# Optimization experiments

Hardware: AMD Instinct MI355X
Metric: run time of the kernel (lower is better)

Reference implementation:

```python
import jax, jax.numpy as jnp
import numpy as np

NPG = 39      # nodes per graph, from (1+8+64+9)*(39+1)=3280 = lin1 in_features
NEG_SLOPE = 0.2


def gat_conv(x, src, dst, W, a_src, a_dst, b, n):
    """PyG GATConv, heads=1, self-loops already appended to (src, dst).
    x:[N,Fin] W:[Fin,Fout] a_src/a_dst:[Fout] b:[Fout] -> [N,Fout]"""
    h = x @ W                                        # [N,Fout]
    e = jax.nn.leaky_relu(h[src] @ a_src + h[dst] @ a_dst, NEG_SLOPE)  # [E]
    m = jax.lax.stop_gradient(jax.ops.segment_max(e, dst, num_segments=n))
    w = jnp.exp(e - m[dst])
    denom = jax.ops.segment_sum(w, dst, num_segments=n)
    alpha = w / (denom[dst] + 1e-16)                 # segment softmax per target node
    out = jax.ops.segment_sum(alpha[:, None] * h[src], dst, num_segments=n)
    return out + b


def setup_inputs() -> dict:
    key = jax.random.key(0)
    ks = jax.random.split(key, 20)
    B, DEG = 4096, 8
    N = B * NPG
    E = N * DEG
    x = jax.random.normal(ks[0], (N, 1), dtype=jnp.float32)
    # block-diagonal edges: each node emits DEG edges to random nodes in SAME graph
    src = jnp.repeat(jnp.arange(N, dtype=jnp.int64), DEG)
    offs = (src // NPG) * NPG
    dst = offs + jax.random.randint(ks[1], (E,), 0, NPG, dtype=jnp.int64)
    edge_index = jnp.stack([src, dst])
    batch_vec = jnp.repeat(jnp.arange(B, dtype=jnp.int64), NPG)

    def glorot(k, shape):
        fan = shape[0] + (shape[1] if len(shape) > 1 else 1)
        s = jnp.sqrt(6.0 / fan)
        return jax.random.uniform(k, shape, jnp.float32, -s, s)

    p = {
        'W1': glorot(ks[2], (1, 8)),   'a1s': glorot(ks[3], (8,)),  'a1d': glorot(ks[4], (8,)),  'b1': jnp.zeros((8,), jnp.float32),
        'W2': glorot(ks[5], (8, 64)),  'a2s': glorot(ks[6], (64,)), 'a2d': glorot(ks[7], (64,)), 'b2': jnp.zeros((64,), jnp.float32),
        'W3': glorot(ks[8], (64, 9)),  'a3s': glorot(ks[9], (9,)),  'a3d': glorot(ks[10], (9,)), 'b3': jnp.zeros((9,), jnp.float32),
        'lW1': glorot(ks[11], (3280, 5000)), 'lb1': jnp.zeros((5000,), jnp.float32),
        'lW2': glorot(ks[12], (5000, 1024)), 'lb2': jnp.zeros((1024,), jnp.float32),
        'lW3': glorot(ks[13], (1024, 9)),    'lb3': jnp.zeros((9,), jnp.float32),
    }
    return {'x': x, 'edge_index': edge_index, 'batch_vec': batch_vec, **p}


def reference(x, edge_index, batch_vec,
              W1, a1s, a1d, b1, W2, a2s, a2d, b2, W3, a3s, a3d, b3,
              lW1, lb1, lW2, lb2, lW3, lb3):
    N = x.shape[0]
    B = N // NPG
    loops = jnp.arange(N, dtype=edge_index.dtype)
    src = jnp.concatenate([edge_index[0], loops])   # GATConv add_self_loops=True
    dst = jnp.concatenate([edge_index[1], loops])

    res = x.reshape(B, -1)                                    # [B,39]
    out0 = jax.ops.segment_max(x, batch_vec, num_segments=B)  # [B,1]

    h1 = jax.nn.relu(gat_conv(x, src, dst, W1, a1s, a1d, b1, N))   # dropout = eval no-op
    res1 = h1.reshape(B, -1)                                   # [B,312]
    out1 = jax.ops.segment_max(h1, batch_vec, num_segments=B)

    h2 = jax.nn.relu(gat_conv(h1, src, dst, W2, a2s, a2d, b2, N))
    res2 = h2.reshape(B, -1)                                   # [B,2496]
    out2 = jax.ops.segment_max(h2, batch_vec, num_segments=B)

    h3 = jax.nn.relu(gat_conv(h2, src, dst, W3, a3s, a3d, b3, N))
    res3 = h3.reshape(B, -1)                                   # [B,351]
    out3 = jax.ops.segment_max(h3, batch_vec, num_segments=B)

    f = jnp.concatenate([res, res1, res2, res3, out0, out1, out2, out3], axis=1)  # [B,3280]
    f = jax.nn.relu(f @ lW1 + lb1)
    f = jax.nn.relu(f @ lW2 + lb2)
    return f @ lW3 + lb3                                       # [B,9]
```

## Files before the change

### kernel.cpp

```cpp
#include <hip/hip_runtime.h>
#include <hip/hip_bf16.h>
#include <stdint.h>


typedef float f32x4 __attribute__((ext_vector_type(4)));
typedef short bf16x8 __attribute__((ext_vector_type(8)));
typedef short s16x4 __attribute__((ext_vector_type(4)));


template<int Fin, int Fout>
__device__ __forceinline__ void gat_layer(
    const float* hin, float* Ht, float* hout,
    const float* __restrict__ W, const float* __restrict__ as_,
    const float* __restrict__ ad_, const float* __restrict__ bias,
    const short* sls, const int* off, float* alpha,
    float* sarr, float* darr, int tid)
{
  for (int idx = tid; idx < 39 * Fout; idx += 256) {
    int i = idx / Fout, f = idx - i * Fout;
    float acc = 0.f;
#pragma unroll
    for (int k = 0; k < Fin; ++k) acc += hin[i * Fin + k] * W[k * Fout + f];
    Ht[idx] = acc;
  }
  __syncthreads();
  if (tid < 39) {
    float s = 0.f, d = 0.f;
    for (int f = 0; f < Fout; ++f) { float h = Ht[tid * Fout + f]; s += h * as_[f]; d += h * ad_[f]; }
    sarr[tid] = s; darr[tid] = d;
  }
  __syncthreads();
  if (tid < 39) {
    int p0 = off[tid], p1 = off[tid + 1];
    float dv = darr[tid];
    float mx = -1e30f;
    for (int p = p0; p < p1; ++p) {
      float e = sarr[sls[p]] + dv;
      e = (e > 0.f) ? e : 0.2f * e;
      alpha[p] = e;
      mx = fmaxf(mx, e);
    }
    float den = 0.f;
    for (int p = p0; p < p1; ++p) { float w = expf(alpha[p] - mx); alpha[p] = w; den += w; }
    float inv = 1.f / (den + 1e-16f);
    for (int p = p0; p < p1; ++p) alpha[p] *= inv;
  }
  __syncthreads();
  for (int idx = tid; idx < 39 * Fout; idx += 256) {
    int i = idx / Fout, f = idx - i * Fout;
    float acc = 0.f;
    int p1 = off[i + 1];
    for (int p = off[i]; p < p1; ++p) acc += alpha[p] * Ht[sls[p] * Fout + f];
    float v = acc + bias[f];
    hout[idx] = (v > 0.f) ? v : 0.f;
  }
  __syncthreads();
}

__global__ __launch_bounds__(256) void gnn_kernel(
    const float* __restrict__ x,
    const int* __restrict__ esrc, const int* __restrict__ edst,
    const float* __restrict__ W1, const float* __restrict__ a1s, const float* __restrict__ a1d, const float* __restrict__ b1,
    const float* __restrict__ W2, const float* __restrict__ a2s, const float* __restrict__ a2d, const float* __restrict__ b2,
    const float* __restrict__ W3, const float* __restrict__ a3s, const float* __restrict__ a3d, const float* __restrict__ b3,
    short* __restrict__ fA)
{
  const int b = blockIdx.x, tid = threadIdx.x;
  __shared__ float feat[3328];
  __shared__ float Ht[39 * 64];
  __shared__ float sarr[39], darr[39];
  __shared__ float alpha[351];
  __shared__ short sls[351];
  __shared__ int off[40];
  __shared__ int cnt[40];
  __shared__ int cur[40];

  float* sx = feat;
  float* h1 = feat + 39;
  float* h2 = feat + 351;
  float* h3 = feat + 2847;

  if (tid < 39) { sx[tid] = x[b * 39 + tid]; cnt[tid] = 0; }
  __syncthreads();

  const int ebase = b * 312;
  for (int e = tid; e < 351; e += 256) {
    int ld = (e < 312) ? (edst[ebase + e] - b * 39) : (e - 312);
    atomicAdd(&cnt[ld], 1);
  }
  __syncthreads();
  if (tid == 0) {
    int s = 0;
    for (int i = 0; i < 39; ++i) { off[i] = s; s += cnt[i]; }
    off[39] = s;
  }
  __syncthreads();
  if (tid < 39) cur[tid] = off[tid];
  __syncthreads();
  for (int e = tid; e < 351; e += 256) {
    int ls, ld;
    if (e < 312) { ls = esrc[ebase + e] - b * 39; ld = edst[ebase + e] - b * 39; }
    else         { ls = e - 312; ld = ls; }
    int p = atomicAdd(&cur[ld], 1);
    sls[p] = (short)ls;
  }
  __syncthreads();

  gat_layer<1, 8 >(sx, Ht, h1, W1, a1s, a1d, b1, sls, off, alpha, sarr, darr, tid);
  gat_layer<8, 64>(h1, Ht, h2, W2, a2s, a2d, b2, sls, off, alpha, sarr, darr, tid);
  gat_layer<64, 9>(h2, Ht, h3, W3, a3s, a3d, b3, sls, off, alpha, sarr, darr, tid);

  if (tid < 82) {
    float mx = -1e30f;
    if (tid == 0) {
      for (int i = 0; i < 39; ++i) mx = fmaxf(mx, sx[i]);
      feat[3198] = mx;
    } else if (tid < 9) {
      int f = tid - 1;
      for (int i = 0; i < 39; ++i) mx = fmaxf(mx, h1[i * 8 + f]);
      feat[3199 + f] = mx;
    } else if (tid < 73) {
      int f = tid - 9;
      for (int i = 0; i < 39; ++i) mx = fmaxf(mx, h2[i * 64 + f]);
      feat[3207 + f] = mx;
    } else {
      int f = tid - 73;
      for (int i = 0; i < 39; ++i) mx = fmaxf(mx, h3[i * 9 + f]);
      feat[3271 + f] = mx;
    }
  }
  for (int c = 3280 + tid; c < 3328; c += 256) feat[c] = 0.f;
  __syncthreads();

  const int rt = b >> 7, mi = (b >> 4) & 7, lrow = b & 15;
  for (int c8 = tid; c8 < 416; c8 += 256) {
    int c = c8 * 8;
    int kt = c >> 6, kq = (c >> 5) & 1, lch = (c >> 3) & 3;
    union { bf16x8 v; __hip_bfloat16 h[8]; } z;
#pragma unroll
    for (int jj = 0; jj < 8; ++jj) z.h[jj] = __float2bfloat16(feat[c + jj]);
    size_t addr = ((((size_t)rt * 52 + kt) * 16) + mi * 2 + kq) * 512 + ((size_t)lrow + 16 * lch) * 8;
    *(bf16x8*)&fA[addr] = z.v;
  }
}


__global__ __launch_bounds__(256) void conv_tiled(
    const float* __restrict__ W, short* __restrict__ WT,
    int K0, int N0, int KT)
{
  __shared__ float t[32][33];
  const int kb = blockIdx.x * 32, nb = blockIdx.y * 32;
  const int tx = threadIdx.x & 31, ty = threadIdx.x >> 5;
#pragma unroll
  for (int i = 0; i < 4; ++i) {
    int k = kb + ty + i * 8, n = nb + tx;
    t[ty + i * 8][tx] = (k < K0 && n < N0) ? W[(size_t)k * N0 + n] : 0.0f;
  }
  __syncthreads();
  const int u = threadIdx.x;
  if (u < 128) {
    int nl = u >> 2, kc = u & 3;
    int n = nb + nl, k = kb + kc * 8;
    union { bf16x8 v; __hip_bfloat16 h[8]; } z;
#pragma unroll
    for (int jj = 0; jj < 8; ++jj) z.h[jj] = __float2bfloat16(t[kc * 8 + jj][nl]);
    int rt = n >> 7, mi = (n >> 4) & 7, lr = n & 15;
    int kt = k >> 6, kq = (k >> 5) & 1, lc = (k >> 3) & 3;
    size_t addr = ((((size_t)rt * KT) + kt) * 16 + mi * 2 + kq) * 512 + ((size_t)lr + 16 * lc) * 8;
    *(bf16x8*)&WT[addr] = z.v;
  }
}


__device__ __forceinline__ void gld_lds16(const void* g, void* l) {
  typedef const __attribute__((address_space(1))) unsigned int GU;
  typedef __attribute__((address_space(3))) unsigned int LU;
  __builtin_amdgcn_global_load_lds((GU*)g, (LU*)l, 16, 0, 0);
}

template<int MODE>
__global__ __launch_bounds__(256) void gemm_tiled(
    const short* __restrict__ A, const short* __restrict__ B,
    const float* __restrict__ bias, int Nreal,
    void* __restrict__ Cout, int Nn, int KT, int ktPerSplit, int outKT)
{
  __shared__ __align__(16) short lA[8192];
  __shared__ __align__(16) short lB[8192];
  const int tid = threadIdx.x;
  const int w = tid >> 6, L = tid & 63;
  const int lrow = L & 15, lch = L >> 4;
  const int mt = blockIdx.y, nt = blockIdx.x;
  const int mw = (w >> 1) * 4, nw = (w & 1) * 4;
  const int kt0 = blockIdx.z * ktPerSplit, kt1 = kt0 + ktPerSplit;

  const short* Ab = A + ((size_t)mt * KT) * 8192 + (size_t)L * 8;
  const short* Bb = B + ((size_t)nt * KT) * 8192 + (size_t)L * 8;

  f32x4 acc[4][4] = {};

  for (int kt = kt0; kt < kt1; ++kt) {
    const short* Ak = Ab + (size_t)kt * 8192;
    const short* Bk = Bb + (size_t)kt * 8192;
#pragma unroll
    for (int j = 0; j < 4; ++j) {
      int st = w * 4 + j;
      gld_lds16(Ak + st * 512, &lA[st * 512]);
      gld_lds16(Bk + st * 512, &lB[st * 512]);
    }
    __syncthreads();
#pragma unroll
    for (int kk = 0; kk < 2; ++kk) {
      bf16x8 af[4], bfr[4];
#pragma unroll
      for (int i = 0; i < 4; ++i) {
        af[i]  = *(const bf16x8*)&lA[((mw + i) * 2 + kk) * 512 + L * 8];
        bfr[i] = *(const bf16x8*)&lB[((nw + i) * 2 + kk) * 512 + L * 8];
      }
#pragma unroll
      for (int i = 0; i < 4; ++i)
#pragma unroll
        for (int j = 0; j < 4; ++j)
          acc[i][j] = __builtin_amdgcn_mfma_f32_16x16x32_bf16(af[i], bfr[j], acc[i][j], 0, 0, 0);
    }
    __syncthreads();
  }

  if (MODE == 0) {
    __hip_bfloat16* C = (__hip_bfloat16*)Cout;
#pragma unroll
    for (int j = 0; j < 4; ++j) {
      int n = nt * 128 + (nw + j) * 16 + lrow;
      float bn = (n < Nreal) ? bias[n] : 0.f;
      int kt = n >> 6, kq = (n >> 5) & 1, lc2 = (n >> 3) & 3, j2 = n & 7;
#pragma unroll
      for (int i = 0; i < 4; ++i) {
        int mi = mw + i;
        size_t base = ((((size_t)mt * outKT + kt) * 16) + mi * 2 + kq) * 512
                      + (size_t)(lch * 4) * 8 + (size_t)lc2 * 128 + j2;
#pragma unroll
        for (int r = 0; r < 4; ++r)
          C[base + r * 8] = __float2bfloat16(fmaxf(acc[i][j][r] + bn, 0.f));
      }
    }
  } else {
    float* P = (float*)Cout + (size_t)blockIdx.z * 4096 * 1024;
#pragma unroll
    for (int j = 0; j < 4; ++j) {
      int n = nt * 128 + (nw + j) * 16 + lrow;
#pragma unroll
      for (int i = 0; i < 4; ++i) {
#pragma unroll
        for (int r = 0; r < 4; ++r) {
          int m = mt * 128 + (mw + i) * 16 + lch * 4 + r;
          P[(size_t)m * Nn + n] = acc[i][j][r];
        }
      }
    }
  }
}


__global__ __launch_bounds__(256) void reduce_k(
    const float* __restrict__ P, const float* __restrict__ bias,
    __hip_bfloat16* __restrict__ C2)
{
  int idx = blockIdx.x * 256 + threadIdx.x;
  const f32x4* p0 = (const f32x4*)P;
  const f32x4* p1 = p0 + (size_t)4096 * 256;
  f32x4 a = p0[idx], b = p1[idx];
  f32x4 bb = ((const f32x4*)bias)[idx & 255];
  union { s16x4 v; __hip_bfloat16 h[4]; } z;
#pragma unroll
  for (int c = 0; c < 4; ++c) z.h[c] = __float2bfloat16(fmaxf(a[c] + b[c] + bb[c], 0.f));
  *(s16x4*)&C2[(size_t)idx * 4] = z.v;
}


__global__ __launch_bounds__(256) void gemm3_kernel(
    const __hip_bfloat16* __restrict__ C2,
    const float* __restrict__ W3,
    const float* __restrict__ b3,
    float* __restrict__ out)
{
  __shared__ float sW3[9 * 1024];
  int tid = threadIdx.x;
  for (int i = tid; i < 9216; i += 256) { int k = i / 9, j = i - 9 * k; sW3[j * 1024 + k] = W3[i]; }
  __syncthreads();
  int row = blockIdx.x * 4 + (tid >> 6);
  int lane = tid & 63;
  const __hip_bfloat16* cr = C2 + (size_t)row * 1024;
  float acc[9] = {0, 0, 0, 0, 0, 0, 0, 0, 0};
  for (int t = 0; t < 16; ++t) {
    int k = lane + 64 * t;
    float c = __bfloat162float(cr[k]);
#pragma unroll
    for (int j = 0; j < 9; ++j) acc[j] += c * sW3[j * 1024 + k];
  }
#pragma unroll
  for (int j = 0; j < 9; ++j) {
    float v = acc[j];
    v += __shfl_down(v, 32, 64);
    v += __shfl_down(v, 16, 64);
    v += __shfl_down(v, 8, 64);
    v += __shfl_down(v, 4, 64);
    v += __shfl_down(v, 2, 64);
    v += __shfl_down(v, 1, 64);
    if (lane == 0) out[(size_t)row * 9 + j] = v + b3[j];
  }
}


extern "C" void kernel_launch(void* const* d_in, const int* in_sizes, int n_in,
                              void* d_out, int out_size, void* d_ws, size_t ws_size,
                              hipStream_t stream)
{
  const float* x   = (const float*)d_in[0];
  const int*   ei  = (const int*)d_in[1];
  const float* W1  = (const float*)d_in[3];
  const float* a1s = (const float*)d_in[4];
  const float* a1d = (const float*)d_in[5];
  const float* b1  = (const float*)d_in[6];
  const float* W2  = (const float*)d_in[7];
  const float* a2s = (const float*)d_in[8];
  const float* a2d = (const float*)d_in[9];
  const float* b2  = (const float*)d_in[10];
  const float* W3  = (const float*)d_in[11];
  const float* a3s = (const float*)d_in[12];
  const float* a3d = (const float*)d_in[13];
  const float* b3  = (const float*)d_in[14];
  const float* lW1 = (const float*)d_in[15];
  const float* lb1 = (const float*)d_in[16];
  const float* lW2 = (const float*)d_in[17];
  const float* lb2 = (const float*)d_in[18];
  const float* lW3 = (const float*)d_in[19];
  const float* lb3 = (const float*)d_in[20];

  const int E = 4096 * 39 * 8;
  const int* esrc = ei;
  const int* edst = ei + E;

  short* fA  = (short*)d_ws;
  short* W1T = fA  + (size_t)4096 * 3328;
  short* C1  = W1T + (size_t)5120 * 3328;
  short* W2T = C1  + (size_t)4096 * 5120;
  float* P = (float*)d_ws;
  __hip_bfloat16* C2 = (__hip_bfloat16*)((float*)d_ws + (size_t)2 * 4096 * 1024);

  conv_tiled<<<dim3(3328 / 32, 5120 / 32), 256, 0, stream>>>(lW1, W1T, 3280, 5000, 52);
  conv_tiled<<<dim3(5120 / 32, 1024 / 32), 256, 0, stream>>>(lW2, W2T, 5000, 1024, 80);
  gnn_kernel<<<4096, 256, 0, stream>>>(x, esrc, edst,
                                       W1, a1s, a1d, b1, W2, a2s, a2d, b2, W3, a3s, a3d, b3, fA);
  gemm_tiled<0><<<dim3(40, 32, 1), 256, 0, stream>>>(fA, W1T, lb1, 5000, C1, 5120, 52, 52, 80);
  gemm_tiled<1><<<dim3(8, 32, 2), 256, 0, stream>>>(C1, W2T, nullptr, 1024, P, 1024, 80, 40, 0);
  reduce_k<<<4096, 256, 0, stream>>>(P, lb2, C2);
  gemm3_kernel<<<1024, 256, 0, stream>>>(C2, lW3, lb3, (float*)d_out);
}
```

Baseline: 531.6 us.

## Rewrite GNN stage as one-wave-per-graph, vectorize weight conversion, fuse split-K reduce into final GEMM

The GAT stage now assigns one 64-lane wavefront per graph (two graphs per 128-thread block). It uses shuffle-based scans and max reductions instead of block barriers, stores intermediates in fp16/bf16 shared memory, and folds softmax normalization into the aggregation. The weight transpose/convert kernel uses 64x64 tiles with float4 loads. The split-K reduce kernel is removed, and the final 1024->9 GEMM reads both fp32 partials directly, applying bias and ReLU inline. The aim is fewer barriers, fewer launches and less intermediate traffic, at the cost of fp16 rounding in the GNN intermediates and reading fp32 partials in the last GEMM.

Result: slower. 554.7 us (+4.3%).

```diff
diff --git a/kernel.cpp b/kernel.cpp
--- a/kernel.cpp
+++ b/kernel.cpp
@@ -1,63 +1,31 @@
 #include <hip/hip_runtime.h>
 #include <hip/hip_bf16.h>
+#include <hip/hip_fp16.h>
 #include <stdint.h>
 
 
 typedef float f32x4 __attribute__((ext_vector_type(4)));
 typedef short bf16x8 __attribute__((ext_vector_type(8)));
-typedef short s16x4 __attribute__((ext_vector_type(4)));
-
-
-template<int Fin, int Fout>
-__device__ __forceinline__ void gat_layer(
-    const float* hin, float* Ht, float* hout,
-    const float* __restrict__ W, const float* __restrict__ as_,
-    const float* __restrict__ ad_, const float* __restrict__ bias,
-    const short* sls, const int* off, float* alpha,
-    float* sarr, float* darr, int tid)
-{
-  for (int idx = tid; idx < 39 * Fout; idx += 256) {
-    int i = idx / Fout, f = idx - i * Fout;
-    float acc = 0.f;
-#pragma unroll
-    for (int k = 0; k < Fin; ++k) acc += hin[i * Fin + k] * W[k * Fout + f];
-    Ht[idx] = acc;
-  }
-  __syncthreads();
-  if (tid < 39) {
-    float s = 0.f, d = 0.f;
-    for (int f = 0; f < Fout; ++f) { float h = Ht[tid * Fout + f]; s += h * as_[f]; d += h * ad_[f]; }
-    sarr[tid] = s; darr[tid] = d;
-  }
-  __syncthreads();
-  if (tid < 39) {
-    int p0 = off[tid], p1 = off[tid + 1];
-    float dv = darr[tid];
+
+
+__device__ __forceinline__ void seg_softmax(
+    float* al, const unsigned short* sl, const int* off, float* sa, float d, int L)
+{
+  if (L < 39) {
+    int p0 = off[L], p1 = off[L + 1];
     float mx = -1e30f;
     for (int p = p0; p < p1; ++p) {
-      float e = sarr[sls[p]] + dv;
+      float e = sa[sl[p]] + d;
       e = (e > 0.f) ? e : 0.2f * e;
-      alpha[p] = e;
-      mx = fmaxf(mx, e);
+      al[p] = e; mx = fmaxf(mx, e);
     }
     float den = 0.f;
-    for (int p = p0; p < p1; ++p) { float w = expf(alpha[p] - mx); alpha[p] = w; den += w; }
-    float inv = 1.f / (den + 1e-16f);
-    for (int p = p0; p < p1; ++p) alpha[p] *= inv;
-  }
-  __syncthreads();
-  for (int idx = tid; idx < 39 * Fout; idx += 256) {
-    int i = idx / Fout, f = idx - i * Fout;
-    float acc = 0.f;
-    int p1 = off[i + 1];
-    for (int p = off[i]; p < p1; ++p) acc += alpha[p] * Ht[sls[p] * Fout + f];
-    float v = acc + bias[f];
-    hout[idx] = (v > 0.f) ? v : 0.f;
-  }
-  __syncthreads();
-}
-
-__global__ __launch_bounds__(256) void gnn_kernel(
+    for (int p = p0; p < p1; ++p) { float wv = __expf(al[p] - mx); al[p] = wv; den += wv; }
+    sa[L] = 1.f / (den + 1e-16f);
+  }
+}
+
+__global__ __launch_bounds__(128) void gnn_wave(
     const float* __restrict__ x,
     const int* __restrict__ esrc, const int* __restrict__ edst,
     const float* __restrict__ W1, const float* __restrict__ a1s, const float* __restrict__ a1d, const float* __restrict__ b1,
@@ -65,82 +33,190 @@
     const float* __restrict__ W3, const float* __restrict__ a3s, const float* __restrict__ a3d, const float* __restrict__ b3,
     short* __restrict__ fA)
 {
-  const int b = blockIdx.x, tid = threadIdx.x;
-  __shared__ float feat[3328];
-  __shared__ float Ht[39 * 64];
-  __shared__ float sarr[39], darr[39];
-  __shared__ float alpha[351];
-  __shared__ short sls[351];
-  __shared__ int off[40];
-  __shared__ int cnt[40];
-  __shared__ int cur[40];
-
-  float* sx = feat;
-  float* h1 = feat + 39;
-  float* h2 = feat + 351;
-  float* h3 = feat + 2847;
-
-  if (tid < 39) { sx[tid] = x[b * 39 + tid]; cnt[tid] = 0; }
+  __shared__ __align__(16) __hip_bfloat16 featA[2][3328];
+  __shared__ __align__(16) __half h2pA[2][2576];
+  __shared__ __align__(16) char HtRawA[2][5152];
+  __shared__ __align__(16) __half h1hA[2][320];
+  __shared__ float alphaA[2][352];
+  __shared__ unsigned short slsA[2][352];
+  __shared__ int offA[2][40];
+  __shared__ int curA[2][40];
+  __shared__ float sarrA[2][40];
+  __shared__ float sW3s[576];
+
+  const int tid = threadIdx.x, w = tid >> 6, L = tid & 63;
+  const int g = blockIdx.x * 2 + w;
+
+  for (int i = tid; i < 576; i += 128) sW3s[i] = W3[i];
   __syncthreads();
 
-  const int ebase = b * 312;
-  for (int e = tid; e < 351; e += 256) {
-    int ld = (e < 312) ? (edst[ebase + e] - b * 39) : (e - 312);
-    atomicAdd(&cnt[ld], 1);
-  }
-  __syncthreads();
-  if (tid == 0) {
-    int s = 0;
-    for (int i = 0; i < 39; ++i) { off[i] = s; s += cnt[i]; }
-    off[39] = s;
-  }
-  __syncthreads();
-  if (tid < 39) cur[tid] = off[tid];
-  __syncthreads();
-  for (int e = tid; e < 351; e += 256) {
-    int ls, ld;
-    if (e < 312) { ls = esrc[ebase + e] - b * 39; ld = edst[ebase + e] - b * 39; }
-    else         { ls = e - 312; ld = ls; }
-    int p = atomicAdd(&cur[ld], 1);
-    sls[p] = (short)ls;
-  }
-  __syncthreads();
-
-  gat_layer<1, 8 >(sx, Ht, h1, W1, a1s, a1d, b1, sls, off, alpha, sarr, darr, tid);
-  gat_layer<8, 64>(h1, Ht, h2, W2, a2s, a2d, b2, sls, off, alpha, sarr, darr, tid);
-  gat_layer<64, 9>(h2, Ht, h3, W3, a3s, a3d, b3, sls, off, alpha, sarr, darr, tid);
-
-  if (tid < 82) {
-    float mx = -1e30f;
-    if (tid == 0) {
-      for (int i = 0; i < 39; ++i) mx = fmaxf(mx, sx[i]);
-      feat[3198] = mx;
-    } else if (tid < 9) {
-      int f = tid - 1;
-      for (int i = 0; i < 39; ++i) mx = fmaxf(mx, h1[i * 8 + f]);
-      feat[3199 + f] = mx;
-    } else if (tid < 73) {
-      int f = tid - 9;
-      for (int i = 0; i < 39; ++i) mx = fmaxf(mx, h2[i * 64 + f]);
-      feat[3207 + f] = mx;
-    } else {
-      int f = tid - 73;
-      for (int i = 0; i < 39; ++i) mx = fmaxf(mx, h3[i * 9 + f]);
-      feat[3271 + f] = mx;
-    }
-  }
-  for (int c = 3280 + tid; c < 3328; c += 256) feat[c] = 0.f;
-  __syncthreads();
-
-  const int rt = b >> 7, mi = (b >> 4) & 7, lrow = b & 15;
-  for (int c8 = tid; c8 < 416; c8 += 256) {
-    int c = c8 * 8;
-    int kt = c >> 6, kq = (c >> 5) & 1, lch = (c >> 3) & 3;
-    union { bf16x8 v; __hip_bfloat16 h[8]; } z;
-#pragma unroll
-    for (int jj = 0; jj < 8; ++jj) z.h[jj] = __float2bfloat16(feat[c + jj]);
-    size_t addr = ((((size_t)rt * 52 + kt) * 16) + mi * 2 + kq) * 512 + ((size_t)lrow + 16 * lch) * 8;
-    *(bf16x8*)&fA[addr] = z.v;
+  __hip_bfloat16* ft = featA[w];
+  __half* hp = h2pA[w];
+  float* Hf = (float*)HtRawA[w];
+  __half* Hh = (__half*)HtRawA[w];
+  __half* h1h = h1hA[w];
+  float* al = alphaA[w];
+  unsigned short* sl = slsA[w];
+  int* off = offA[w]; int* cur = curA[w];
+  float* sa = sarrA[w];
+
+  float xv = 0.f;
+  if (L < 39) { xv = x[g * 39 + L]; ft[L] = __float2bfloat16(xv); }
+  {
+    float m = (L < 39) ? xv : -1e30f;
+    for (int o = 32; o >= 1; o >>= 1) m = fmaxf(m, __shfl_xor(m, o, 64));
+    if (L == 0) ft[3198] = __float2bfloat16(m);
+  }
+
+  if (L < 39) cur[L] = 0;
+  int els[6], eld[6];
+  const int eb = g * 312, nb0 = g * 39;
+#pragma unroll
+  for (int it = 0; it < 6; ++it) {
+    int e = it * 64 + L;
+    int ls = 0, ld = 0;
+    bool v = e < 351;
+    if (v) {
+      if (e < 312) { ls = esrc[eb + e] - nb0; ld = edst[eb + e] - nb0; }
+      else         { ls = e - 312; ld = ls; }
+      atomicAdd(&cur[ld], 1);
+    }
+    els[it] = v ? ls : -1; eld[it] = ld;
+  }
+  int c = (L < 39) ? cur[L] : 0;
+  int incl = c;
+  for (int o = 1; o < 64; o <<= 1) { int t = __shfl_up(incl, o, 64); if (L >= o) incl += t; }
+  if (L < 39) { off[L] = incl - c; cur[L] = incl - c; }
+  if (L == 38) off[39] = incl;
+#pragma unroll
+  for (int it = 0; it < 6; ++it)
+    if (els[it] >= 0) { int p = atomicAdd(&cur[eld[it]], 1); sl[p] = (unsigned short)els[it]; }
+
+  {
+    const int fi = L & 7, ni = L >> 3;
+    float w1v = W1[fi], b1v = b1[fi];
+#pragma unroll
+    for (int it = 0; it < 5; ++it) {
+      int i = it * 8 + ni;
+      if (i < 39) Hf[i * 9 + fi] = __shfl(xv, i, 64) * w1v;
+    }
+    {
+      int row = (L < 39) ? L : 0;
+      float s = 0.f, d = 0.f;
+#pragma unroll
+      for (int f = 0; f < 8; ++f) { float h = Hf[row * 9 + f]; s += h * a1s[f]; d += h * a1d[f]; }
+      if (L < 39) sa[L] = s;
+      seg_softmax(al, sl, off, sa, d, L);
+    }
+    float m1 = -1e30f;
+#pragma unroll
+    for (int it = 0; it < 5; ++it) {
+      int i = it * 8 + ni;
+      if (i < 39) {
+        float acc = 0.f;
+        int p1 = off[i + 1];
+        for (int p = off[i]; p < p1; ++p) acc += al[p] * Hf[sl[p] * 9 + fi];
+        float v = fmaxf(acc * sa[i] + b1v, 0.f);
+        ft[39 + i * 8 + fi] = __float2bfloat16(v);
+        h1h[i * 8 + fi] = __float2half(v);
+        m1 = fmaxf(m1, v);
+      }
+    }
+    m1 = fmaxf(m1, __shfl_xor(m1, 8, 64));
+    m1 = fmaxf(m1, __shfl_xor(m1, 16, 64));
+    m1 = fmaxf(m1, __shfl_xor(m1, 32, 64));
+    if (L < 8) ft[3199 + L] = __float2bfloat16(m1);
+  }
+
+  {
+    float w2k[8];
+#pragma unroll
+    for (int k = 0; k < 8; ++k) w2k[k] = W2[k * 64 + L];
+    float a2sv = a2s[L], a2dv = a2d[L], b2v = b2[L];
+    for (int i = 0; i < 39; ++i) {
+      float hv = 0.f;
+#pragma unroll
+      for (int k = 0; k < 8; ++k) hv += __half2float(h1h[i * 8 + k]) * w2k[k];
+      Hh[i * 66 + L] = __float2half(hv);
+    }
+    {
+      int row = (L < 39) ? L : 0;
+      float s = 0.f, d = 0.f;
+      for (int f = 0; f < 64; ++f) {
+        float h = __half2float(Hh[row * 66 + f]);
+        s += h * __shfl(a2sv, f, 64); d += h * __shfl(a2dv, f, 64);
+      }
+      if (L < 39) sa[L] = s;
+      seg_softmax(al, sl, off, sa, d, L);
+    }
+    float m2 = -1e30f;
+    for (int i = 0; i < 39; ++i) {
+      float acc = 0.f;
+      int p0 = off[i], p1 = off[i + 1];
+      for (int p = p0; p < p1; ++p) acc += al[p] * __half2float(Hh[sl[p] * 66 + L]);
+      float v = fmaxf(acc * sa[i] + b2v, 0.f);
+      ft[351 + i * 64 + L] = __float2bfloat16(v);
+      hp[i * 66 + L] = __float2half(v);
+      m2 = fmaxf(m2, v);
+    }
+    ft[3207 + L] = __float2bfloat16(m2);
+  }
+
+  {
+    const int i7 = L / 9, f3 = L - 9 * i7;
+    const bool act = L < 63;
+    float b3v = act ? b3[f3] : 0.f;
+#pragma unroll
+    for (int it = 0; it < 6; ++it) {
+      int i = it * 7 + i7;
+      if (act && i < 39) {
+        float acc = 0.f;
+        for (int k = 0; k < 64; ++k) acc += __half2float(hp[i * 66 + k]) * sW3s[k * 9 + f3];
+        Hf[i * 10 + f3] = acc;
+      }
+    }
+    {
+      int row = (L < 39) ? L : 0;
+      float s = 0.f, d = 0.f;
+#pragma unroll
+      for (int f = 0; f < 9; ++f) { float h = Hf[row * 10 + f]; s += h * a3s[f]; d += h * a3d[f]; }
+      if (L < 39) sa[L] = s;
+      seg_softmax(al, sl, off, sa, d, L);
+    }
+#pragma unroll
+    for (int it = 0; it < 6; ++it) {
+      int i = it * 7 + i7;
+      if (act && i < 39) {
+        float acc = 0.f;
+        int p1 = off[i + 1];
+        for (int p = off[i]; p < p1; ++p) acc += al[p] * Hf[sl[p] * 10 + f3];
+        float v = fmaxf(acc * sa[i] + b3v, 0.f);
+        ft[2847 + i * 9 + f3] = __float2bfloat16(v);
+      }
+    }
+    if (L < 9) {
+      float m = -1e30f;
+      for (int i = 0; i < 39; ++i) m = fmaxf(m, __bfloat162float(ft[2847 + i * 9 + L]));
+      ft[3271 + L] = __float2bfloat16(m);
+    }
+    if (L < 48) ft[3280 + L] = __float2bfloat16(0.f);
+  }
+
+  {
+    const int rt = g >> 7, mi = (g >> 4) & 7, lrow = g & 15;
+    const size_t rowbase = (size_t)rt * 52 * 8192;
+#pragma unroll
+    for (int it = 0; it < 7; ++it) {
+      int c8 = it * 64 + L;
+      if (c8 < 416) {
+        int cc = c8 * 8;
+        int kt = cc >> 6, kq = (cc >> 5) & 1, lch = (cc >> 3) & 3;
+        bf16x8 v = *(const bf16x8*)&ft[cc];
+        size_t addr = rowbase + (size_t)kt * 8192 + (size_t)(mi * 2 + kq) * 512
+                    + (size_t)(lrow + 16 * lch) * 8;
+        *(bf16x8*)&fA[addr] = v;
+      }
+    }
   }
 }
 
@@ -149,22 +225,27 @@
     const float* __restrict__ W, short* __restrict__ WT,
     int K0, int N0, int KT)
 {
-  __shared__ float t[32][33];
-  const int kb = blockIdx.x * 32, nb = blockIdx.y * 32;
-  const int tx = threadIdx.x & 31, ty = threadIdx.x >> 5;
-#pragma unroll
-  for (int i = 0; i < 4; ++i) {
-    int k = kb + ty + i * 8, n = nb + tx;
-    t[ty + i * 8][tx] = (k < K0 && n < N0) ? W[(size_t)k * N0 + n] : 0.0f;
+  __shared__ float t[64][68];
+  const int kb = blockIdx.x * 64, nb = blockIdx.y * 64;
+  const int tid = threadIdx.x;
+  const int tx = tid & 15, ty = tid >> 4;
+#pragma unroll
+  for (int r = 0; r < 4; ++r) {
+    int k = kb + ty + r * 16, n = nb + tx * 4;
+    float4 v = make_float4(0.f, 0.f, 0.f, 0.f);
+    if (k < K0 && n < N0) v = *(const float4*)&W[(size_t)k * N0 + n];
+    t[ty + r * 16][tx * 4 + 0] = v.x; t[ty + r * 16][tx * 4 + 1] = v.y;
+    t[ty + r * 16][tx * 4 + 2] = v.z; t[ty + r * 16][tx * 4 + 3] = v.w;
   }
   __syncthreads();
-  const int u = threadIdx.x;
-  if (u < 128) {
-    int nl = u >> 2, kc = u & 3;
+  const int nl = tid >> 2, kc0 = tid & 3;
+#pragma unroll
+  for (int h = 0; h < 2; ++h) {
+    int kc = kc0 + h * 4;
     int n = nb + nl, k = kb + kc * 8;
-    union { bf16x8 v; __hip_bfloat16 h[8]; } z;
-#pragma unroll
-    for (int jj = 0; jj < 8; ++jj) z.h[jj] = __float2bfloat16(t[kc * 8 + jj][nl]);
+    union { bf16x8 v; __hip_bfloat16 b[8]; } z;
+#pragma unroll
+    for (int j = 0; j < 8; ++j) z.b[j] = __float2bfloat16(t[kc * 8 + j][nl]);
     int rt = n >> 7, mi = (n >> 4) & 7, lr = n & 15;
     int kt = k >> 6, kq = (k >> 5) & 1, lc = (k >> 3) & 3;
     size_t addr = ((((size_t)rt * KT) + kt) * 16 + mi * 2 + kq) * 512 + ((size_t)lr + 16 * lc) * 8;
@@ -173,10 +254,10 @@
 }
 
 
-__device__ __forceinline__ void gld_lds16(const void* g, void* l) {
+__device__ __forceinline__ void gld_lds16(const void* gptr, void* l) {
   typedef const __attribute__((address_space(1))) unsigned int GU;
   typedef __attribute__((address_space(3))) unsigned int LU;
-  __builtin_amdgcn_global_load_lds((GU*)g, (LU*)l, 16, 0, 0);
+  __builtin_amdgcn_global_load_lds((GU*)gptr, (LU*)l, 16, 0, 0);
 }
 
 template<int MODE>
@@ -249,38 +330,22 @@
     for (int j = 0; j < 4; ++j) {
       int n = nt * 128 + (nw + j) * 16 + lrow;
 #pragma unroll
-      for (int i = 0; i < 4; ++i) {
+      for (int i = 0; i < 4; ++i)
 #pragma unroll
         for (int r = 0; r < 4; ++r) {
           int m = mt * 128 + (mw + i) * 16 + lch * 4 + r;
           P[(size_t)m * Nn + n] = acc[i][j][r];
         }
-      }
-    }
-  }
-}
-
-
-__global__ __launch_bounds__(256) void reduce_k(
-    const float* __restrict__ P, const float* __restrict__ bias,
-    __hip_bfloat16* __restrict__ C2)
-{
-  int idx = blockIdx.x * 256 + threadIdx.x;
-  const f32x4* p0 = (const f32x4*)P;
-  const f32x4* p1 = p0 + (size_t)4096 * 256;
-  f32x4 a = p0[idx], b = p1[idx];
-  f32x4 bb = ((const f32x4*)bias)[idx & 255];
-  union { s16x4 v; __hip_bfloat16 h[4]; } z;
-#pragma unroll
-  for (int c = 0; c < 4; ++c) z.h[c] = __float2bfloat16(fmaxf(a[c] + b[c] + bb[c], 0.f));
-  *(s16x4*)&C2[(size_t)idx * 4] = z.v;
-}
-
-
-__global__ __launch_bounds__(256) void gemm3_kernel(
-    const __hip_bfloat16* __restrict__ C2,
+    }
+  }
+}
+
+
+__global__ __launch_bounds__(256) void gemm3_fused(
+    const float* __restrict__ P,
+    const float* __restrict__ b2v,
     const float* __restrict__ W3,
-    const float* __restrict__ b3,
+    const float* __restrict__ b3v,
     float* __restrict__ out)
 {
   __shared__ float sW3[9 * 1024];
@@ -289,11 +354,12 @@
   __syncthreads();
   int row = blockIdx.x * 4 + (tid >> 6);
   int lane = tid & 63;
-  const __hip_bfloat16* cr = C2 + (size_t)row * 1024;
+  const float* p0 = P + (size_t)row * 1024;
+  const float* p1 = p0 + (size_t)4096 * 1024;
   float acc[9] = {0, 0, 0, 0, 0, 0, 0, 0, 0};
   for (int t = 0; t < 16; ++t) {
     int k = lane + 64 * t;
-    float c = __bfloat162float(cr[k]);
+    float c = fmaxf(p0[k] + p1[k] + b2v[k], 0.f);
 #pragma unroll
     for (int j = 0; j < 9; ++j) acc[j] += c * sW3[j * 1024 + k];
   }
@@ -306,7 +372,7 @@
     v += __shfl_down(v, 4, 64);
     v += __shfl_down(v, 2, 64);
     v += __shfl_down(v, 1, 64);
-    if (lane == 0) out[(size_t)row * 9 + j] = v + b3[j];
+    if (lane == 0) out[(size_t)row * 9 + j] = v + b3v[j];
   }
 }
 
@@ -344,15 +410,13 @@
   short* W1T = fA  + (size_t)4096 * 3328;
   short* C1  = W1T + (size_t)5120 * 3328;
   short* W2T = C1  + (size_t)4096 * 5120;
-  float* P = (float*)d_ws;
-  __hip_bfloat16* C2 = (__hip_bfloat16*)((float*)d_ws + (size_t)2 * 4096 * 1024);
-
-  conv_tiled<<<dim3(3328 / 32, 5120 / 32), 256, 0, stream>>>(lW1, W1T, 3280, 5000, 52);
-  conv_tiled<<<dim3(5120 / 32, 1024 / 32), 256, 0, stream>>>(lW2, W2T, 5000, 1024, 80);
-  gnn_kernel<<<4096, 256, 0, stream>>>(x, esrc, edst,
-                                       W1, a1s, a1d, b1, W2, a2s, a2d, b2, W3, a3s, a3d, b3, fA);
+  float* P   = (float*)d_ws;
+
+  conv_tiled<<<dim3(3328 / 64, 5120 / 64), 256, 0, stream>>>(lW1, W1T, 3280, 5000, 52);
+  conv_tiled<<<dim3(5120 / 64, 1024 / 64), 256, 0, stream>>>(lW2, W2T, 5000, 1024, 80);
+  gnn_wave<<<2048, 128, 0, stream>>>(x, esrc, edst,
+                                     W1, a1s, a1d, b1, W2, a2s, a2d, b2, W3, a3s, a3d, b3, fA);
   gemm_tiled<0><<<dim3(40, 32, 1), 256, 0, stream>>>(fA, W1T, lb1, 5000, C1, 5120, 52, 52, 80);
   gemm_tiled<1><<<dim3(8, 32, 2), 256, 0, stream>>>(C1, W2T, nullptr, 1024, P, 1024, 80, 40, 0);
-  reduce_k<<<4096, 256, 0, stream>>>(P, lb2, C2);
-  gemm3_kernel<<<1024, 256, 0, stream>>>(C2, lW3, lb3, (float*)d_out);
-}
+  gemm3_fused<<<1024, 256, 0, stream>>>(P, lb2, lW3, lb3, (float*)d_out);
+}
```
